# Kernel tuning notes

Measured on AMD Instinct MI355X. Metric: run time of the kernel, lower is better.

Reference implementation:

```python
import jax, jax.numpy as jnp
import numpy as np

OUT_FEATURES = 4096
IN_FEATURES = 4096
GROUP_SIZE = 128
NUM_GROUPS = OUT_FEATURES // GROUP_SIZE  # groups along output-channel axis (axis=0)


def _unpack_int8_to_int4(packed, num_elements):
    # Each int8 byte holds two signed int4 values: low nibble first, then high nibble.
    p = packed.astype(jnp.int8)
    low = jnp.right_shift(jnp.left_shift(p, 4), 4)   # sign-extended low nibble, in [-8, 7]
    high = jnp.right_shift(p, 4)                      # arithmetic shift -> sign-extended high nibble
    vals = jnp.stack([low, high], axis=-1).reshape(-1)
    return vals[:num_elements]


def _dequantize_weight(packed_weight, scales, zero_points):
    int4 = _unpack_int8_to_int4(packed_weight, OUT_FEATURES * IN_FEATURES)
    w = int4.astype(jnp.float32).reshape(NUM_GROUPS, GROUP_SIZE, IN_FEATURES)
    # per-group (over output channels): (q - zp) * scale
    w = (w - zero_points[:, None, None]) * scales[:, None, None]
    return w.reshape(OUT_FEATURES, IN_FEATURES)


def setup_inputs() -> dict:
    key = jax.random.key(0)
    k_x, k_w, k_s, k_zp, k_b = jax.random.split(key, 5)
    x = jax.random.normal(k_x, (8192, IN_FEATURES), dtype=jnp.float32)
    # packed int4 weights stored as signed bytes
    packed_weight = jax.random.randint(k_w, (OUT_FEATURES * IN_FEATURES // 2,), 0, 256, dtype=jnp.int32) - 128
    scales = jax.random.uniform(k_s, (NUM_GROUPS,), dtype=jnp.float32) * 0.02 + 0.001
    zero_points = jax.random.normal(k_zp, (NUM_GROUPS,), dtype=jnp.float32) * 0.5
    bias = jax.random.normal(k_b, (OUT_FEATURES,), dtype=jnp.float32)
    return {"x": x, "packed_weight": packed_weight, "scales": scales,
            "zero_points": zero_points, "bias": bias}


def reference(x, packed_weight, scales, zero_points, bias):
    weight = _dequantize_weight(packed_weight, scales, zero_points)  # [out, in]
    return jnp.einsum('bi,oi->bo', x, weight) + bias
```

## Files before the change

### kernel.cpp

```cpp
#include <hip/hip_runtime.h>
#include <cstdint>
#include <cstddef>

#define M_DIM 8192
#define N_DIM 4096
#define K_DIM 4096
#define CHUNK_M 4096

typedef __attribute__((ext_vector_type(8))) short bf16x8;
typedef __attribute__((ext_vector_type(4))) float floatx4;

__device__ __forceinline__ ushort f2bf_rne(float f) {
    union { float f; uint32_t u; } a;
    a.f = f;
    uint32_t u = a.u;
    uint32_t r = (u + 0x7fffu + ((u >> 16) & 1u)) >> 16;
    return (ushort)r;
}

__device__ __forceinline__ uint32_t pk_bf_trunc(float f0, float f1) {
    return __builtin_amdgcn_perm(__float_as_uint(f1), __float_as_uint(f0),
                                 0x07060302u);
}

__global__ void dequant_w_kernel(const int4* __restrict__ pw,
                                 const float* __restrict__ scales,
                                 const float* __restrict__ zps,
                                 uint4* __restrict__ wb, int np4) {
    int p4 = blockIdx.x * blockDim.x + threadIdx.x;
    if (p4 >= np4) return;
    int p = p4 * 4;
    int g = p >> 18;
    float s = scales[g];
    float b = -zps[g] * s;
    int4 v = pw[p4];
    int vv[4] = { v.x, v.y, v.z, v.w };
    ushort o[8];
#pragma unroll
    for (int j = 0; j < 4; ++j) {
        int lo = ((int)((uint32_t)vv[j] << 28)) >> 28;
        int hi = ((int)((uint32_t)vv[j] << 24)) >> 28;
        o[2 * j]     = f2bf_rne(fmaf((float)lo, s, b));
        o[2 * j + 1] = f2bf_rne(fmaf((float)hi, s, b));
    }
    uint4 st;
    st.x = (uint32_t)o[0] | ((uint32_t)o[1] << 16);
    st.y = (uint32_t)o[2] | ((uint32_t)o[3] << 16);
    st.z = (uint32_t)o[4] | ((uint32_t)o[5] << 16);
    st.w = (uint32_t)o[6] | ((uint32_t)o[7] << 16);
    wb[p4] = st;
}

__global__ void convert_x_kernel(const float4* __restrict__ x4,
                                 ushort4* __restrict__ out4, int n4) {
    int i = blockIdx.x * blockDim.x + threadIdx.x;
    if (i >= n4) return;
    float4 v = x4[i];
    ushort4 o;
    o.x = f2bf_rne(v.x);
    o.y = f2bf_rne(v.y);
    o.z = f2bf_rne(v.z);
    o.w = f2bf_rne(v.w);
    out4[i] = o;
}

#define TBM 256
#define TBN 256
#define TBK 32
#define NT  (K_DIM / TBK)
#define A_E 8192
#define SLOT_E 16384

__global__ __launch_bounds__(512, 2)
void gemm_bf16_256(const ushort* __restrict__ A,
                   const ushort* __restrict__ B,
                   const float* __restrict__ bias,
                   float* __restrict__ C) {
    __shared__ ushort lds[4 * SLOT_E];

    const int tid  = threadIdx.x;
    const int lane = tid & 63;
    const int wave = tid >> 6;
    const int wm   = wave >> 2;
    const int wn   = wave & 3;

    const int nwg = gridDim.x;
    const int cpx = nwg >> 3;
    const int bid = blockIdx.x;
    const int swz = (bid & 7) * cpx + (bid >> 3);
    const int bn  = swz & (N_DIM / TBN - 1);
    const int bm  = swz / (N_DIM / TBN);

    const ushort* Ab = A + (size_t)(bm * TBM) * K_DIM;
    const ushort* Bb = B + (size_t)(bn * TBN) * K_DIM;

    const int srow = tid >> 2;
    const int scol = (((tid & 3) ^ ((tid >> 3) & 3)) * 8);
    const ushort* gA0 = Ab + (size_t)srow * K_DIM + scol;
    const ushort* gA1 = gA0 + (size_t)128 * K_DIM;
    const ushort* gB0 = Bb + (size_t)srow * K_DIM + scol;
    const ushort* gB1 = gB0 + (size_t)128 * K_DIM;
    const int wdst = wave * 512;

    const int frow = lane & 15;
    const int fcol = (((lane >> 4) ^ ((frow >> 1) & 3)) * 8);
    const int aoff = (wm * 128 + frow) * TBK + fcol;
    const int boff = A_E + (wn * 64 + frow) * TBK + fcol;

    floatx4 acc[8][4] = {};

#define STAGE_A(tt)                                                           \
    {                                                                          \
        const int k0s = ((tt) & (NT - 1)) * TBK;                               \
        ushort* d = lds + ((tt) & 3) * SLOT_E + wdst;                          \
        __builtin_amdgcn_global_load_lds(                                      \
            (const __attribute__((address_space(1))) void*)(gA0 + k0s),        \
            (__attribute__((address_space(3))) void*)d, 16, 0, 0);             \
        __builtin_amdgcn_global_load_lds(                                      \
            (const __attribute__((address_space(1))) void*)(gA1 + k0s),        \
            (__attribute__((address_space(3))) void*)(d + 4096), 16, 0, 0);    \
    }
#define STAGE_B(tt)                                                           \
    {                                                                          \
        const int k0s = ((tt) & (NT - 1)) * TBK;                               \
        ushort* d = lds + ((tt) & 3) * SLOT_E + A_E + wdst;                    \
        __builtin_amdgcn_global_load_lds(                                      \
            (const __attribute__((address_space(1))) void*)(gB0 + k0s),        \
            (__attribute__((address_space(3))) void*)d, 16, 0, 0);             \
        __builtin_amdgcn_global_load_lds(                                      \
            (const __attribute__((address_space(1))) void*)(gB1 + k0s),        \
            (__attribute__((address_space(3))) void*)(d + 4096), 16, 0, 0);    \
    }

#define BODY(T, afc, bfc, afn, bfn)                                           \
    {                                                                          \
        const ushort* bcur = lds + ((T) & 3) * SLOT_E;                         \
        const ushort* bnxt = lds + (((T) + 1) & 3) * SLOT_E;                   \
        bf16x8 afb[4];                                                         \
                                             \
        _Pragma("unroll")                                                      \
        for (int i = 0; i < 4; ++i)                                            \
            afb[i] = *(const bf16x8*)(bcur + aoff + (4 + i) * 512);            \
        STAGE_A((T) + 3)                                                       \
        __builtin_amdgcn_sched_barrier(0);                                     \
        __builtin_amdgcn_s_setprio(1);                                         \
        _Pragma("unroll")                                                      \
        for (int i = 0; i < 2; ++i)                                            \
            _Pragma("unroll")                                                  \
            for (int j = 0; j < 4; ++j)                                        \
                acc[i][j] = __builtin_amdgcn_mfma_f32_16x16x32_bf16(           \
                    afc[i], bfc[j], acc[i][j], 0, 0, 0);                       \
        __builtin_amdgcn_s_setprio(0);                                         \
        __builtin_amdgcn_sched_barrier(0);                                     \
                                             \
        _Pragma("unroll")                                                      \
        for (int j = 0; j < 4; ++j)                                            \
            bfn[j] = *(const bf16x8*)(bnxt + boff + j * 512);                  \
        STAGE_B((T) + 3)                                                       \
        __builtin_amdgcn_sched_barrier(0);                                     \
        __builtin_amdgcn_s_setprio(1);                                         \
        _Pragma("unroll")                                                      \
        for (int i = 2; i < 4; ++i)                                            \
            _Pragma("unroll")                                                  \
            for (int j = 0; j < 4; ++j)                                        \
                acc[i][j] = __builtin_amdgcn_mfma_f32_16x16x32_bf16(           \
                    afc[i], bfc[j], acc[i][j], 0, 0, 0);                       \
        __builtin_amdgcn_s_setprio(0);                                         \
        __builtin_amdgcn_sched_barrier(0);                                     \
                                                            \
        _Pragma("unroll")                                                      \
        for (int i = 0; i < 4; ++i)                                            \
            afn[i] = *(const bf16x8*)(bnxt + aoff + i * 512);                  \
        __builtin_amdgcn_sched_barrier(0);                                     \
                \
        asm volatile("s_waitcnt lgkmcnt(8)" ::: "memory");                     \
        __builtin_amdgcn_sched_barrier(0);                                     \
        __builtin_amdgcn_s_setprio(1);                                         \
        _Pragma("unroll")                                                      \
        for (int i = 0; i < 2; ++i)                                            \
            _Pragma("unroll")                                                  \
            for (int j = 0; j < 4; ++j)                                        \
                acc[4 + i][j] = __builtin_amdgcn_mfma_f32_16x16x32_bf16(       \
                    afb[i], bfc[j], acc[4 + i][j], 0, 0, 0);                   \
        __builtin_amdgcn_s_setprio(0);                                         \
        __builtin_amdgcn_sched_barrier(0);                                     \
        __builtin_amdgcn_s_setprio(1);                                         \
        _Pragma("unroll")                                                      \
        for (int i = 2; i < 4; ++i)                                            \
            _Pragma("unroll")                                                  \
            for (int j = 0; j < 4; ++j)                                        \
                acc[4 + i][j] = __builtin_amdgcn_mfma_f32_16x16x32_bf16(       \
                    afb[i], bfc[j], acc[4 + i][j], 0, 0, 0);                   \
        __builtin_amdgcn_s_setprio(0);                                         \
        asm volatile("s_waitcnt vmcnt(4)" ::: "memory");                       \
        __builtin_amdgcn_s_barrier();                                          \
        __builtin_amdgcn_sched_barrier(0);                                     \
    }

    STAGE_A(0) STAGE_B(0)
    STAGE_A(1) STAGE_B(1)
    STAGE_A(2) STAGE_B(2)
    asm volatile("s_waitcnt vmcnt(4)" ::: "memory");
    __builtin_amdgcn_s_barrier();
    __builtin_amdgcn_sched_barrier(0);

    bf16x8 af0[4], bf0[4], af1[4], bf1[4];
#pragma unroll
    for (int j = 0; j < 4; ++j)
        bf0[j] = *(const bf16x8*)(lds + boff + j * 512);
#pragma unroll
    for (int i = 0; i < 4; ++i)
        af0[i] = *(const bf16x8*)(lds + aoff + i * 512);

    for (int t = 0; t < NT; t += 2) {
        BODY(t,     af0, bf0, af1, bf1)
        BODY(t + 1, af1, bf1, af0, bf0)
    }
#undef BODY
#undef STAGE_A
#undef STAGE_B

    const int crow0 = bm * TBM + wm * 128;
    const int ccol0 = bn * TBN + wn * 64;
    const int rl = lane >> 4;
    const int cl = lane & 15;
#pragma unroll
    for (int j = 0; j < 4; ++j) {
        const int col = ccol0 + j * 16 + cl;
        const float bv = bias[col];
#pragma unroll
        for (int i = 0; i < 8; ++i) {
            const int row = crow0 + i * 16 + rl * 4;
            float* cp = C + (size_t)row * N_DIM + col;
#pragma unroll
            for (int r = 0; r < 4; ++r)
                cp[(size_t)r * N_DIM] = acc[i][j][r] + bv;
        }
    }
}

#define BM 128
#define BN 128
#define BK 32

__global__ void gemm_fused_kernel(const float* __restrict__ X,
                                  const ushort* __restrict__ B,
                                  const float* __restrict__ bias,
                                  float* __restrict__ C) {
    __shared__ ushort As[BM * BK];
    __shared__ ushort Bs[BN * BK];

    const int tid  = threadIdx.x;
    const int lane = tid & 63;
    const int wave = tid >> 6;
    const int wm   = wave >> 1;
    const int wn   = wave & 1;
    const int bm   = blockIdx.y;
    const int bn   = blockIdx.x;

    const int ar = tid >> 2;
    const int ac = (tid & 3) * 8;
    const float* xp0 = X + (size_t)(bm * BM + ar) * K_DIM + ac;
    const float* xp1 = xp0 + (size_t)64 * K_DIM;
    ushort* as0 = As + ar * BK + ac;
    ushort* as1 = as0 + 64 * BK;

    const int scol = (lane & 3) * 8;
    const ushort* Bb = B + (size_t)(bn * BN) * K_DIM;

    floatx4 acc[4][4] = {};

    for (int k0 = 0; k0 < K_DIM; k0 += BK) {
        float4 a0 = *(const float4*)(xp0 + k0);
        float4 a1 = *(const float4*)(xp0 + k0 + 4);
        float4 b0 = *(const float4*)(xp1 + k0);
        float4 b1 = *(const float4*)(xp1 + k0 + 4);
#pragma unroll
        for (int q = 0; q < 2; ++q) {
            const int chunk = wave * 2 + q;
            const int r = chunk * 16 + (lane >> 2);
            const ushort* gb = Bb + (size_t)r * K_DIM + k0 + scol;
            __builtin_amdgcn_global_load_lds(
                (const __attribute__((address_space(1))) void*)gb,
                (__attribute__((address_space(3))) void*)(Bs + chunk * 512),
                16, 0, 0);
        }
        uint4 w0, w1;
        w0.x = pk_bf_trunc(a0.x, a0.y);
        w0.y = pk_bf_trunc(a0.z, a0.w);
        w0.z = pk_bf_trunc(a1.x, a1.y);
        w0.w = pk_bf_trunc(a1.z, a1.w);
        w1.x = pk_bf_trunc(b0.x, b0.y);
        w1.y = pk_bf_trunc(b0.z, b0.w);
        w1.z = pk_bf_trunc(b1.x, b1.y);
        w1.w = pk_bf_trunc(b1.z, b1.w);
        *(uint4*)as0 = w0;
        *(uint4*)as1 = w1;

        __syncthreads();

        bf16x8 af[4], bfr[4];
        const int frow = lane & 15;
        const int fcol = (lane >> 4) * 8;
#pragma unroll
        for (int i = 0; i < 4; ++i) {
            af[i]  = *(const bf16x8*)(As + (wm * 64 + i * 16 + frow) * BK + fcol);
            bfr[i] = *(const bf16x8*)(Bs + (wn * 64 + i * 16 + frow) * BK + fcol);
        }
#pragma unroll
        for (int i = 0; i < 4; ++i)
#pragma unroll
            for (int j = 0; j < 4; ++j)
                acc[i][j] = __builtin_amdgcn_mfma_f32_16x16x32_bf16(
                    af[i], bfr[j], acc[i][j], 0, 0, 0);
        __syncthreads();
    }

    const int crow0 = bm * BM + wm * 64;
    const int ccol0 = bn * BN + wn * 64;
    const int rl = lane >> 4;
    const int cl = lane & 15;
#pragma unroll
    for (int j = 0; j < 4; ++j) {
        const int col = ccol0 + j * 16 + cl;
        const float bv = bias[col];
#pragma unroll
        for (int i = 0; i < 4; ++i) {
            const int row = crow0 + i * 16 + rl * 4;
            float* cp = C + (size_t)row * N_DIM + col;
#pragma unroll
            for (int r = 0; r < 4; ++r)
                cp[(size_t)r * N_DIM] = acc[i][j][r] + bv;
        }
    }
}

extern "C" void kernel_launch(void* const* d_in, const int* in_sizes, int n_in,
                              void* d_out, int out_size, void* d_ws, size_t ws_size,
                              hipStream_t stream) {
    const float* x      = (const float*)d_in[0];
    const int*   pw     = (const int*)d_in[1];
    const float* scales = (const float*)d_in[2];
    const float* zps    = (const float*)d_in[3];
    const float* bias   = (const float*)d_in[4];
    float* out = (float*)d_out;

    ushort* wb = (ushort*)d_ws;

    {
        int np4 = (N_DIM * K_DIM / 2) / 4;
        dequant_w_kernel<<<np4 / 256, 256, 0, stream>>>(
            (const int4*)pw, scales, zps, (uint4*)wb, np4);
    }

    const size_t need_full  = ((size_t)N_DIM * K_DIM + (size_t)M_DIM * K_DIM) * 2;
    const size_t need_chunk = ((size_t)N_DIM * K_DIM + (size_t)CHUNK_M * K_DIM) * 2;

    if (ws_size >= need_full) {
        ushort* xb = wb + (size_t)N_DIM * K_DIM;
        int n4 = (M_DIM * K_DIM) / 4;
        convert_x_kernel<<<n4 / 256, 256, 0, stream>>>(
            (const float4*)x, (ushort4*)xb, n4);
        int nblk = (M_DIM / TBM) * (N_DIM / TBN);
        gemm_bf16_256<<<nblk, 512, 0, stream>>>(xb, wb, bias, out);
    } else if (ws_size >= need_chunk) {
        ushort* xb = wb + (size_t)N_DIM * K_DIM;
        for (int c = 0; c < M_DIM / CHUNK_M; ++c) {
            const float* xc = x + (size_t)c * CHUNK_M * K_DIM;
            float* oc = out + (size_t)c * CHUNK_M * N_DIM;
            int n4 = (CHUNK_M * K_DIM) / 4;
            convert_x_kernel<<<n4 / 256, 256, 0, stream>>>(
                (const float4*)xc, (ushort4*)xb, n4);
            int nblk = (CHUNK_M / TBM) * (N_DIM / TBN);
            gemm_bf16_256<<<nblk, 512, 0, stream>>>(xb, wb, bias, oc);
        }
    } else {
        dim3 grid(N_DIM / BN, M_DIM / BM);
        gemm_fused_kernel<<<grid, 256, 0, stream>>>(x, wb, bias, out);
    }
}
```

Before: 464.3 us.

## Restructure bf16 GEMM main loop to TBK=64 double-buffered quadrant schedule

Reworks the 256x256 bf16 GEMM from a 4-slot TBK=32 ring into a 2-buffer TBK=64 scheme. Each K tile is split into four MFMA quadrants (A lo/hi by B lo/hi), and the next tile's global-to-LDS loads are interleaved between them. Wave-to-output mapping changes to split rows and columns into two halves, and the LDS swizzle widens to 8 chunks. The aim is fewer barriers per FLOP and more MFMA work per LDS fetch, at the cost of more barriers inside each tile and a shallower prefetch depth.

```diff
diff --git a/kernel.cpp b/kernel.cpp
--- a/kernel.cpp
+++ b/kernel.cpp
@@ -66,17 +66,16 @@
 
 #define TBM 256
 #define TBN 256
-#define TBK 32
-#define NT  (K_DIM / TBK)
-#define A_E 8192
-#define SLOT_E 16384
+#define TBK 64
+#define NKT (K_DIM / TBK)
+#define BUF_E 32768
 
 __global__ __launch_bounds__(512, 2)
 void gemm_bf16_256(const ushort* __restrict__ A,
                    const ushort* __restrict__ B,
                    const float* __restrict__ bias,
                    float* __restrict__ C) {
-    __shared__ ushort lds[4 * SLOT_E];
+    __shared__ ushort lds[2 * BUF_E];
 
     const int tid  = threadIdx.x;
     const int lane = tid & 63;
@@ -94,143 +93,149 @@
     const ushort* Ab = A + (size_t)(bm * TBM) * K_DIM;
     const ushort* Bb = B + (size_t)(bn * TBN) * K_DIM;
 
-    const int srow = tid >> 2;
-    const int scol = (((tid & 3) ^ ((tid >> 3) & 3)) * 8);
-    const ushort* gA0 = Ab + (size_t)srow * K_DIM + scol;
-    const ushort* gA1 = gA0 + (size_t)128 * K_DIM;
-    const ushort* gB0 = Bb + (size_t)srow * K_DIM + scol;
-    const ushort* gB1 = gB0 + (size_t)128 * K_DIM;
-    const int wdst = wave * 512;
+    const int r0 = tid >> 3;
+    const int kc = ((tid & 7) ^ (r0 & 7)) * 8;
+    const ushort* gA = Ab + (size_t)r0 * K_DIM + kc;
+    const ushort* gB = Bb + (size_t)r0 * K_DIM + kc;
+    const int sdst = tid * 8;
 
     const int frow = lane & 15;
-    const int fcol = (((lane >> 4) ^ ((frow >> 1) & 3)) * 8);
-    const int aoff = (wm * 128 + frow) * TBK + fcol;
-    const int boff = A_E + (wn * 64 + frow) * TBK + fcol;
+    const int col0 = (((lane >> 4) ^ (frow & 7)) * 8);
+    const int lbA = wm * 4096 + frow * 64;
+    const int lbB = 16384 + wn * 2048 + frow * 64;
+    const int colx[2] = { col0, col0 ^ 32 };
 
     floatx4 acc[8][4] = {};
 
-#define STAGE_A(tt)                                                           \
+#define STAGE(SBUF, TS, OFFE, ROWOFF)                                         \
     {                                                                          \
-        const int k0s = ((tt) & (NT - 1)) * TBK;                               \
-        ushort* d = lds + ((tt) & 3) * SLOT_E + wdst;                          \
+        const int k0s = ((TS) & (NKT - 1)) * TBK;                              \
+        ushort* d = (ushort*)lds + (SBUF) * BUF_E + (OFFE) + sdst;             \
+        const ushort* g = ((OFFE) >= 16384 ? gB : gA);                         \
         __builtin_amdgcn_global_load_lds(                                      \
-            (const __attribute__((address_space(1))) void*)(gA0 + k0s),        \
+            (const __attribute__((address_space(1))) void*)                    \
+                (g + (size_t)(ROWOFF) * K_DIM + k0s),                          \
             (__attribute__((address_space(3))) void*)d, 16, 0, 0);             \
         __builtin_amdgcn_global_load_lds(                                      \
-            (const __attribute__((address_space(1))) void*)(gA1 + k0s),        \
+            (const __attribute__((address_space(1))) void*)                    \
+                (g + (size_t)((ROWOFF) + 64) * K_DIM + k0s),                   \
             (__attribute__((address_space(3))) void*)(d + 4096), 16, 0, 0);    \
     }
-#define STAGE_B(tt)                                                           \
+
+#define MFMA_Q(ILO, AFR, JLO, BFR)                                            \
+    _Pragma("unroll")                                                          \
+    for (int i = 0; i < 4; ++i)                                                \
+        _Pragma("unroll")                                                      \
+        for (int j = 0; j < 2; ++j)                                            \
+            _Pragma("unroll")                                                  \
+            for (int ks = 0; ks < 2; ++ks)                                     \
+                acc[(ILO) + i][(JLO) + j] =                                    \
+                    __builtin_amdgcn_mfma_f32_16x16x32_bf16(                   \
+                        AFR[i][ks], BFR[j][ks], acc[(ILO) + i][(JLO) + j],     \
+                        0, 0, 0);
+
+#define TILE(T, CBUF)                                                         \
     {                                                                          \
-        const int k0s = ((tt) & (NT - 1)) * TBK;                               \
-        ushort* d = lds + ((tt) & 3) * SLOT_E + A_E + wdst;                    \
-        __builtin_amdgcn_global_load_lds(                                      \
-            (const __attribute__((address_space(1))) void*)(gB0 + k0s),        \
-            (__attribute__((address_space(3))) void*)d, 16, 0, 0);             \
-        __builtin_amdgcn_global_load_lds(                                      \
-            (const __attribute__((address_space(1))) void*)(gB1 + k0s),        \
-            (__attribute__((address_space(3))) void*)(d + 4096), 16, 0, 0);    \
-    }
-
-#define BODY(T, afc, bfc, afn, bfn)                                           \
-    {                                                                          \
-        const ushort* bcur = lds + ((T) & 3) * SLOT_E;                         \
-        const ushort* bnxt = lds + (((T) + 1) & 3) * SLOT_E;                   \
-        bf16x8 afb[4];                                                         \
-                                             \
+        bf16x8 alo[4][2], ahi[4][2], blo[2][2], bhi[2][2];                     \
+                                                         \
         _Pragma("unroll")                                                      \
         for (int i = 0; i < 4; ++i)                                            \
-            afb[i] = *(const bf16x8*)(bcur + aoff + (4 + i) * 512);            \
-        STAGE_A((T) + 3)                                                       \
+            _Pragma("unroll")                                                  \
+            for (int ks = 0; ks < 2; ++ks)                                     \
+                alo[i][ks] = *(const bf16x8*)(lds + (CBUF) * BUF_E + lbA +     \
+                                              i * 1024 + colx[ks]);            \
+        _Pragma("unroll")                                                      \
+        for (int j = 0; j < 2; ++j)                                            \
+            _Pragma("unroll")                                                  \
+            for (int ks = 0; ks < 2; ++ks)                                     \
+                blo[j][ks] = *(const bf16x8*)(lds + (CBUF) * BUF_E + lbB +     \
+                                              j * 1024 + colx[ks]);            \
+        STAGE((CBUF) ^ 1, (T) + 1, 0, 0)                                       \
+        asm volatile("s_waitcnt lgkmcnt(8)" ::: "memory");                     \
+        __builtin_amdgcn_s_barrier();                                          \
+        asm volatile("s_waitcnt lgkmcnt(0)" ::: "memory");                     \
         __builtin_amdgcn_sched_barrier(0);                                     \
         __builtin_amdgcn_s_setprio(1);                                         \
-        _Pragma("unroll")                                                      \
-        for (int i = 0; i < 2; ++i)                                            \
-            _Pragma("unroll")                                                  \
-            for (int j = 0; j < 4; ++j)                                        \
-                acc[i][j] = __builtin_amdgcn_mfma_f32_16x16x32_bf16(           \
-                    afc[i], bfc[j], acc[i][j], 0, 0, 0);                       \
-        __builtin_amdgcn_s_setprio(0);                                         \
-        __builtin_amdgcn_sched_barrier(0);                                     \
-                                             \
-        _Pragma("unroll")                                                      \
-        for (int j = 0; j < 4; ++j)                                            \
-            bfn[j] = *(const bf16x8*)(bnxt + boff + j * 512);                  \
-        STAGE_B((T) + 3)                                                       \
-        __builtin_amdgcn_sched_barrier(0);                                     \
-        __builtin_amdgcn_s_setprio(1);                                         \
-        _Pragma("unroll")                                                      \
-        for (int i = 2; i < 4; ++i)                                            \
-            _Pragma("unroll")                                                  \
-            for (int j = 0; j < 4; ++j)                                        \
-                acc[i][j] = __builtin_amdgcn_mfma_f32_16x16x32_bf16(           \
-                    afc[i], bfc[j], acc[i][j], 0, 0, 0);                       \
-        __builtin_amdgcn_s_setprio(0);                                         \
-        __builtin_amdgcn_sched_barrier(0);                                     \
-                                                            \
-        _Pragma("unroll")                                                      \
-        for (int i = 0; i < 4; ++i)                                            \
-            afn[i] = *(const bf16x8*)(bnxt + aoff + i * 512);                  \
-        __builtin_amdgcn_sched_barrier(0);                                     \
-                \
-        asm volatile("s_waitcnt lgkmcnt(8)" ::: "memory");                     \
-        __builtin_amdgcn_sched_barrier(0);                                     \
-        __builtin_amdgcn_s_setprio(1);                                         \
-        _Pragma("unroll")                                                      \
-        for (int i = 0; i < 2; ++i)                                            \
-            _Pragma("unroll")                                                  \
-            for (int j = 0; j < 4; ++j)                                        \
-                acc[4 + i][j] = __builtin_amdgcn_mfma_f32_16x16x32_bf16(       \
-                    afb[i], bfc[j], acc[4 + i][j], 0, 0, 0);                   \
-        __builtin_amdgcn_s_setprio(0);                                         \
-        __builtin_amdgcn_sched_barrier(0);                                     \
-        __builtin_amdgcn_s_setprio(1);                                         \
-        _Pragma("unroll")                                                      \
-        for (int i = 2; i < 4; ++i)                                            \
-            _Pragma("unroll")                                                  \
-            for (int j = 0; j < 4; ++j)                                        \
-                acc[4 + i][j] = __builtin_amdgcn_mfma_f32_16x16x32_bf16(       \
-                    afb[i], bfc[j], acc[4 + i][j], 0, 0, 0);                   \
+        MFMA_Q(0, alo, 0, blo)                                                 \
         __builtin_amdgcn_s_setprio(0);                                         \
         asm volatile("s_waitcnt vmcnt(4)" ::: "memory");                       \
         __builtin_amdgcn_s_barrier();                                          \
         __builtin_amdgcn_sched_barrier(0);                                     \
-    }
-
-    STAGE_A(0) STAGE_B(0)
-    STAGE_A(1) STAGE_B(1)
-    STAGE_A(2) STAGE_B(2)
+                                                         \
+        _Pragma("unroll")                                                      \
+        for (int j = 0; j < 2; ++j)                                            \
+            _Pragma("unroll")                                                  \
+            for (int ks = 0; ks < 2; ++ks)                                     \
+                bhi[j][ks] = *(const bf16x8*)(lds + (CBUF) * BUF_E + lbB +     \
+                                              8192 + j * 1024 + colx[ks]);     \
+        STAGE((CBUF) ^ 1, (T) + 1, 16384, 0)                                   \
+        __builtin_amdgcn_s_barrier();                                          \
+        asm volatile("s_waitcnt lgkmcnt(0)" ::: "memory");                     \
+        __builtin_amdgcn_sched_barrier(0);                                     \
+        __builtin_amdgcn_s_setprio(1);                                         \
+        MFMA_Q(0, alo, 2, bhi)                                                 \
+        __builtin_amdgcn_s_setprio(0);                                         \
+        asm volatile("s_waitcnt vmcnt(4)" ::: "memory");                       \
+        __builtin_amdgcn_s_barrier();                                          \
+        __builtin_amdgcn_sched_barrier(0);                                     \
+                                                         \
+        _Pragma("unroll")                                                      \
+        for (int i = 0; i < 4; ++i)                                            \
+            _Pragma("unroll")                                                  \
+            for (int ks = 0; ks < 2; ++ks)                                     \
+                ahi[i][ks] = *(const bf16x8*)(lds + (CBUF) * BUF_E + lbA +     \
+                                              8192 + i * 1024 + colx[ks]);     \
+        STAGE((CBUF) ^ 1, (T) + 1, 24576, 128)                                 \
+        __builtin_amdgcn_s_barrier();                                          \
+        asm volatile("s_waitcnt lgkmcnt(0)" ::: "memory");                     \
+        __builtin_amdgcn_sched_barrier(0);                                     \
+        __builtin_amdgcn_s_setprio(1);                                         \
+        MFMA_Q(4, ahi, 0, blo)                                                 \
+        __builtin_amdgcn_s_setprio(0);                                         \
+        __builtin_amdgcn_s_barrier();                                          \
+        __builtin_amdgcn_sched_barrier(0);                                     \
+                                                         \
+        STAGE((CBUF) ^ 1, (T) + 1, 8192, 128)                                  \
+        __builtin_amdgcn_s_barrier();                                          \
+        __builtin_amdgcn_sched_barrier(0);                                     \
+        __builtin_amdgcn_s_setprio(1);                                         \
+        MFMA_Q(4, ahi, 2, bhi)                                                 \
+        __builtin_amdgcn_s_setprio(0);                                         \
+        asm volatile("s_waitcnt vmcnt(4)" ::: "memory");                       \
+        __builtin_amdgcn_s_barrier();                                          \
+        __builtin_amdgcn_sched_barrier(0);                                     \
+    }
+
+    STAGE(0, 0, 0, 0)
+    STAGE(0, 0, 16384, 0)
+    STAGE(0, 0, 24576, 128)
+    STAGE(0, 0, 8192, 128)
     asm volatile("s_waitcnt vmcnt(4)" ::: "memory");
     __builtin_amdgcn_s_barrier();
     __builtin_amdgcn_sched_barrier(0);
 
-    bf16x8 af0[4], bf0[4], af1[4], bf1[4];
-#pragma unroll
-    for (int j = 0; j < 4; ++j)
-        bf0[j] = *(const bf16x8*)(lds + boff + j * 512);
-#pragma unroll
-    for (int i = 0; i < 4; ++i)
-        af0[i] = *(const bf16x8*)(lds + aoff + i * 512);
-
-    for (int t = 0; t < NT; t += 2) {
-        BODY(t,     af0, bf0, af1, bf1)
-        BODY(t + 1, af1, bf1, af0, bf0)
-    }
-#undef BODY
-#undef STAGE_A
-#undef STAGE_B
-
-    const int crow0 = bm * TBM + wm * 128;
-    const int ccol0 = bn * TBN + wn * 64;
+    for (int t = 0; t < NKT; t += 2) {
+        TILE(t, 0)
+        TILE(t + 1, 1)
+    }
+#undef TILE
+#undef MFMA_Q
+#undef STAGE
+
     const int rl = lane >> 4;
     const int cl = lane & 15;
 #pragma unroll
     for (int j = 0; j < 4; ++j) {
-        const int col = ccol0 + j * 16 + cl;
+        const int col = bn * TBN +
+                        (j < 2 ? wn * 32 + j * 16 : 128 + wn * 32 + (j - 2) * 16) +
+                        cl;
         const float bv = bias[col];
 #pragma unroll
         for (int i = 0; i < 8; ++i) {
-            const int row = crow0 + i * 16 + rl * 4;
+            const int row = bm * TBM +
+                            (i < 4 ? wm * 64 + i * 16
+                                   : 128 + wm * 64 + (i - 4) * 16) +
+                            rl * 4;
             float* cp = C + (size_t)row * N_DIM + col;
 #pragma unroll
             for (int r = 0; r < 4; ++r)
```

After: 459.3 us. Within noise of the previous version (-1.1%).

## Fuse fp32-to-bf16 activation conversion into the 256x256 GEMM pipeline

Applied to the files above, without the earlier changes.

Removes the separate convert_x kernel and the bf16 copy of x. The GEMM now loads fp32 x straight from global memory into registers, converts it with v_cvt_pk_bf16_f32, and writes it into swizzled LDS, interleaved with the asynchronous B tile loads. This drops a full read and write pass over the 128MB activation and a kernel launch. In exchange the GEMM reads twice as many A bytes per tile through registers instead of direct-to-LDS loads, which adds VGPR pressure and vmcnt synchronisation inside the pipelined main loop. The workspace-size fallback paths are also removed.

```diff
diff --git a/kernel.cpp b/kernel.cpp
--- a/kernel.cpp
+++ b/kernel.cpp
@@ -5,7 +5,6 @@
 #define M_DIM 8192
 #define N_DIM 4096
 #define K_DIM 4096
-#define CHUNK_M 4096
 
 typedef __attribute__((ext_vector_type(8))) short bf16x8;
 typedef __attribute__((ext_vector_type(4))) float floatx4;
@@ -18,9 +17,10 @@
     return (ushort)r;
 }
 
-__device__ __forceinline__ uint32_t pk_bf_trunc(float f0, float f1) {
-    return __builtin_amdgcn_perm(__float_as_uint(f1), __float_as_uint(f0),
-                                 0x07060302u);
+__device__ __forceinline__ uint32_t cvtpk_bf16(float lo, float hi) {
+    uint32_t r;
+    asm("v_cvt_pk_bf16_f32 %0, %1, %2" : "=v"(r) : "v"(lo), "v"(hi));
+    return r;
 }
 
 __global__ void dequant_w_kernel(const int4* __restrict__ pw,
@@ -51,19 +51,6 @@
     wb[p4] = st;
 }
 
-__global__ void convert_x_kernel(const float4* __restrict__ x4,
-                                 ushort4* __restrict__ out4, int n4) {
-    int i = blockIdx.x * blockDim.x + threadIdx.x;
-    if (i >= n4) return;
-    float4 v = x4[i];
-    ushort4 o;
-    o.x = f2bf_rne(v.x);
-    o.y = f2bf_rne(v.y);
-    o.z = f2bf_rne(v.z);
-    o.w = f2bf_rne(v.w);
-    out4[i] = o;
-}
-
 #define TBM 256
 #define TBN 256
 #define TBK 32
@@ -72,10 +59,10 @@
 #define SLOT_E 16384
 
 __global__ __launch_bounds__(512, 2)
-void gemm_bf16_256(const ushort* __restrict__ A,
-                   const ushort* __restrict__ B,
-                   const float* __restrict__ bias,
-                   float* __restrict__ C) {
+void gemm_fused_256(const float* __restrict__ X,
+                    const ushort* __restrict__ B,
+                    const float* __restrict__ bias,
+                    float* __restrict__ C) {
     __shared__ ushort lds[4 * SLOT_E];
 
     const int tid  = threadIdx.x;
@@ -91,16 +78,20 @@
     const int bn  = swz & (N_DIM / TBN - 1);
     const int bm  = swz / (N_DIM / TBN);
 
-    const ushort* Ab = A + (size_t)(bm * TBM) * K_DIM;
     const ushort* Bb = B + (size_t)(bn * TBN) * K_DIM;
 
     const int srow = tid >> 2;
-    const int scol = (((tid & 3) ^ ((tid >> 3) & 3)) * 8);
-    const ushort* gA0 = Ab + (size_t)srow * K_DIM + scol;
-    const ushort* gA1 = gA0 + (size_t)128 * K_DIM;
-    const ushort* gB0 = Bb + (size_t)srow * K_DIM + scol;
+    const int scolB = (((tid & 3) ^ ((tid >> 3) & 3)) * 8);
+    const ushort* gB0 = Bb + (size_t)srow * K_DIM + scolB;
     const ushort* gB1 = gB0 + (size_t)128 * K_DIM;
     const int wdst = wave * 512;
+
+    const int wrow = tid >> 1;
+    const int wh   = tid & 1;
+    const int wq   = (wrow >> 1) & 3;
+    const int we1  = wrow * TBK + (((2 * wh) ^ wq) * 8);
+    const int we2  = we1 ^ 8;
+    const float* gX = X + (size_t)(bm * TBM + wrow) * K_DIM + wh * 16;
 
     const int frow = lane & 15;
     const int fcol = (((lane >> 4) ^ ((frow >> 1) & 3)) * 8);
@@ -108,22 +99,31 @@
     const int boff = A_E + (wn * 64 + frow) * TBK + fcol;
 
     floatx4 acc[8][4] = {};
-
-#define STAGE_A(tt)                                                           \
+    float4 rA0, rA1, rA2, rA3;
+
+#define LOAD_A(tt)                                                            \
+    {                                                                          \
+        const int k0n = ((tt) & (NT - 1)) * TBK;                               \
+        rA0 = *(const float4*)(gX + k0n);                                      \
+        rA1 = *(const float4*)(gX + k0n + 4);                                  \
+        rA2 = *(const float4*)(gX + k0n + 8);                                  \
+        rA3 = *(const float4*)(gX + k0n + 12);                                 \
+    }
+#define WRITE_A(tt)                                                           \
+    {                                                                          \
+        ushort* wp = (ushort*)lds + ((tt) & 3) * SLOT_E;                       \
+        uint4 v1, v2;                                                          \
+        v1.x = cvtpk_bf16(rA0.x, rA0.y); v1.y = cvtpk_bf16(rA0.z, rA0.w);      \
+        v1.z = cvtpk_bf16(rA1.x, rA1.y); v1.w = cvtpk_bf16(rA1.z, rA1.w);      \
+        v2.x = cvtpk_bf16(rA2.x, rA2.y); v2.y = cvtpk_bf16(rA2.z, rA2.w);      \
+        v2.z = cvtpk_bf16(rA3.x, rA3.y); v2.w = cvtpk_bf16(rA3.z, rA3.w);      \
+        *(uint4*)(wp + we1) = v1;                                              \
+        *(uint4*)(wp + we2) = v2;                                              \
+    }
+#define STAGE_B(tt)                                                           \
     {                                                                          \
         const int k0s = ((tt) & (NT - 1)) * TBK;                               \
-        ushort* d = lds + ((tt) & 3) * SLOT_E + wdst;                          \
-        __builtin_amdgcn_global_load_lds(                                      \
-            (const __attribute__((address_space(1))) void*)(gA0 + k0s),        \
-            (__attribute__((address_space(3))) void*)d, 16, 0, 0);             \
-        __builtin_amdgcn_global_load_lds(                                      \
-            (const __attribute__((address_space(1))) void*)(gA1 + k0s),        \
-            (__attribute__((address_space(3))) void*)(d + 4096), 16, 0, 0);    \
-    }
-#define STAGE_B(tt)                                                           \
-    {                                                                          \
-        const int k0s = ((tt) & (NT - 1)) * TBK;                               \
-        ushort* d = lds + ((tt) & 3) * SLOT_E + A_E + wdst;                    \
+        ushort* d = (ushort*)lds + ((tt) & 3) * SLOT_E + A_E + wdst;           \
         __builtin_amdgcn_global_load_lds(                                      \
             (const __attribute__((address_space(1))) void*)(gB0 + k0s),        \
             (__attribute__((address_space(3))) void*)d, 16, 0, 0);             \
@@ -134,14 +134,20 @@
 
 #define BODY(T, afc, bfc, afn, bfn)                                           \
     {                                                                          \
+                \
+        asm volatile("s_waitcnt vmcnt(2)" ::: "memory");                       \
+        __builtin_amdgcn_sched_barrier(0);                                     \
+        WRITE_A((T) + 2)                                                       \
+        LOAD_A((T) + 3)                                                        \
+        __builtin_amdgcn_sched_barrier(0);                                     \
         const ushort* bcur = lds + ((T) & 3) * SLOT_E;                         \
         const ushort* bnxt = lds + (((T) + 1) & 3) * SLOT_E;                   \
         bf16x8 afb[4];                                                         \
-                                             \
+                                                  \
         _Pragma("unroll")                                                      \
         for (int i = 0; i < 4; ++i)                                            \
             afb[i] = *(const bf16x8*)(bcur + aoff + (4 + i) * 512);            \
-        STAGE_A((T) + 3)                                                       \
+        STAGE_B((T) + 3)                                                       \
         __builtin_amdgcn_sched_barrier(0);                                     \
         __builtin_amdgcn_s_setprio(1);                                         \
         _Pragma("unroll")                                                      \
@@ -152,11 +158,10 @@
                     afc[i], bfc[j], acc[i][j], 0, 0, 0);                       \
         __builtin_amdgcn_s_setprio(0);                                         \
         __builtin_amdgcn_sched_barrier(0);                                     \
-                                             \
+                                                            \
         _Pragma("unroll")                                                      \
         for (int j = 0; j < 4; ++j)                                            \
             bfn[j] = *(const bf16x8*)(bnxt + boff + j * 512);                  \
-        STAGE_B((T) + 3)                                                       \
         __builtin_amdgcn_sched_barrier(0);                                     \
         __builtin_amdgcn_s_setprio(1);                                         \
         _Pragma("unroll")                                                      \
@@ -172,7 +177,8 @@
         for (int i = 0; i < 4; ++i)                                            \
             afn[i] = *(const bf16x8*)(bnxt + aoff + i * 512);                  \
         __builtin_amdgcn_sched_barrier(0);                                     \
-                \
+        \
+         \
         asm volatile("s_waitcnt lgkmcnt(8)" ::: "memory");                     \
         __builtin_amdgcn_sched_barrier(0);                                     \
         __builtin_amdgcn_s_setprio(1);                                         \
@@ -192,15 +198,20 @@
                 acc[4 + i][j] = __builtin_amdgcn_mfma_f32_16x16x32_bf16(       \
                     afb[i], bfc[j], acc[4 + i][j], 0, 0, 0);                   \
         __builtin_amdgcn_s_setprio(0);                                         \
-        asm volatile("s_waitcnt vmcnt(4)" ::: "memory");                       \
         __builtin_amdgcn_s_barrier();                                          \
         __builtin_amdgcn_sched_barrier(0);                                     \
     }
 
-    STAGE_A(0) STAGE_B(0)
-    STAGE_A(1) STAGE_B(1)
-    STAGE_A(2) STAGE_B(2)
+    LOAD_A(0)
+    asm volatile("s_waitcnt vmcnt(0)" ::: "memory");
+    WRITE_A(0)
+    LOAD_A(1)
+    asm volatile("s_waitcnt vmcnt(0)" ::: "memory");
+    WRITE_A(1)
+    LOAD_A(2)
+    STAGE_B(0) STAGE_B(1) STAGE_B(2)
     asm volatile("s_waitcnt vmcnt(4)" ::: "memory");
+    asm volatile("s_waitcnt lgkmcnt(0)" ::: "memory");
     __builtin_amdgcn_s_barrier();
     __builtin_amdgcn_sched_barrier(0);
 
@@ -217,8 +228,9 @@
         BODY(t + 1, af1, bf1, af0, bf0)
     }
 #undef BODY
-#undef STAGE_A
 #undef STAGE_B
+#undef WRITE_A
+#undef LOAD_A
 
     const int crow0 = bm * TBM + wm * 128;
     const int ccol0 = bn * TBN + wn * 64;
@@ -230,102 +242,6 @@
         const float bv = bias[col];
 #pragma unroll
         for (int i = 0; i < 8; ++i) {
-            const int row = crow0 + i * 16 + rl * 4;
-            float* cp = C + (size_t)row * N_DIM + col;
-#pragma unroll
-            for (int r = 0; r < 4; ++r)
-                cp[(size_t)r * N_DIM] = acc[i][j][r] + bv;
-        }
-    }
-}
-
-#define BM 128
-#define BN 128
-#define BK 32
-
-__global__ void gemm_fused_kernel(const float* __restrict__ X,
-                                  const ushort* __restrict__ B,
-                                  const float* __restrict__ bias,
-                                  float* __restrict__ C) {
-    __shared__ ushort As[BM * BK];
-    __shared__ ushort Bs[BN * BK];
-
-    const int tid  = threadIdx.x;
-    const int lane = tid & 63;
-    const int wave = tid >> 6;
-    const int wm   = wave >> 1;
-    const int wn   = wave & 1;
-    const int bm   = blockIdx.y;
-    const int bn   = blockIdx.x;
-
-    const int ar = tid >> 2;
-    const int ac = (tid & 3) * 8;
-    const float* xp0 = X + (size_t)(bm * BM + ar) * K_DIM + ac;
-    const float* xp1 = xp0 + (size_t)64 * K_DIM;
-    ushort* as0 = As + ar * BK + ac;
-    ushort* as1 = as0 + 64 * BK;
-
-    const int scol = (lane & 3) * 8;
-    const ushort* Bb = B + (size_t)(bn * BN) * K_DIM;
-
-    floatx4 acc[4][4] = {};
-
-    for (int k0 = 0; k0 < K_DIM; k0 += BK) {
-        float4 a0 = *(const float4*)(xp0 + k0);
-        float4 a1 = *(const float4*)(xp0 + k0 + 4);
-        float4 b0 = *(const float4*)(xp1 + k0);
-        float4 b1 = *(const float4*)(xp1 + k0 + 4);
-#pragma unroll
-        for (int q = 0; q < 2; ++q) {
-            const int chunk = wave * 2 + q;
-            const int r = chunk * 16 + (lane >> 2);
-            const ushort* gb = Bb + (size_t)r * K_DIM + k0 + scol;
-            __builtin_amdgcn_global_load_lds(
-                (const __attribute__((address_space(1))) void*)gb,
-                (__attribute__((address_space(3))) void*)(Bs + chunk * 512),
-                16, 0, 0);
-        }
-        uint4 w0, w1;
-        w0.x = pk_bf_trunc(a0.x, a0.y);
-        w0.y = pk_bf_trunc(a0.z, a0.w);
-        w0.z = pk_bf_trunc(a1.x, a1.y);
-        w0.w = pk_bf_trunc(a1.z, a1.w);
-        w1.x = pk_bf_trunc(b0.x, b0.y);
-        w1.y = pk_bf_trunc(b0.z, b0.w);
-        w1.z = pk_bf_trunc(b1.x, b1.y);
-        w1.w = pk_bf_trunc(b1.z, b1.w);
-        *(uint4*)as0 = w0;
-        *(uint4*)as1 = w1;
-
-        __syncthreads();
-
-        bf16x8 af[4], bfr[4];
-        const int frow = lane & 15;
-        const int fcol = (lane >> 4) * 8;
-#pragma unroll
-        for (int i = 0; i < 4; ++i) {
-            af[i]  = *(const bf16x8*)(As + (wm * 64 + i * 16 + frow) * BK + fcol);
-            bfr[i] = *(const bf16x8*)(Bs + (wn * 64 + i * 16 + frow) * BK + fcol);
-        }
-#pragma unroll
-        for (int i = 0; i < 4; ++i)
-#pragma unroll
-            for (int j = 0; j < 4; ++j)
-                acc[i][j] = __builtin_amdgcn_mfma_f32_16x16x32_bf16(
-                    af[i], bfr[j], acc[i][j], 0, 0, 0);
-        __syncthreads();
-    }
-
-    const int crow0 = bm * BM + wm * 64;
-    const int ccol0 = bn * BN + wn * 64;
-    const int rl = lane >> 4;
-    const int cl = lane & 15;
-#pragma unroll
-    for (int j = 0; j < 4; ++j) {
-        const int col = ccol0 + j * 16 + cl;
-        const float bv = bias[col];
-#pragma unroll
-        for (int i = 0; i < 4; ++i) {
             const int row = crow0 + i * 16 + rl * 4;
             float* cp = C + (size_t)row * N_DIM + col;
 #pragma unroll
@@ -353,29 +269,6 @@
             (const int4*)pw, scales, zps, (uint4*)wb, np4);
     }
 
-    const size_t need_full  = ((size_t)N_DIM * K_DIM + (size_t)M_DIM * K_DIM) * 2;
-    const size_t need_chunk = ((size_t)N_DIM * K_DIM + (size_t)CHUNK_M * K_DIM) * 2;
-
-    if (ws_size >= need_full) {
-        ushort* xb = wb + (size_t)N_DIM * K_DIM;
-        int n4 = (M_DIM * K_DIM) / 4;
-        convert_x_kernel<<<n4 / 256, 256, 0, stream>>>(
-            (const float4*)x, (ushort4*)xb, n4);
-        int nblk = (M_DIM / TBM) * (N_DIM / TBN);
-        gemm_bf16_256<<<nblk, 512, 0, stream>>>(xb, wb, bias, out);
-    } else if (ws_size >= need_chunk) {
-        ushort* xb = wb + (size_t)N_DIM * K_DIM;
-        for (int c = 0; c < M_DIM / CHUNK_M; ++c) {
-            const float* xc = x + (size_t)c * CHUNK_M * K_DIM;
-            float* oc = out + (size_t)c * CHUNK_M * N_DIM;
-            int n4 = (CHUNK_M * K_DIM) / 4;
-            convert_x_kernel<<<n4 / 256, 256, 0, stream>>>(
-                (const float4*)xc, (ushort4*)xb, n4);
-            int nblk = (CHUNK_M / TBM) * (N_DIM / TBN);
-            gemm_bf16_256<<<nblk, 512, 0, stream>>>(xb, wb, bias, oc);
-        }
-    } else {
-        dim3 grid(N_DIM / BN, M_DIM / BM);
-        gemm_fused_kernel<<<grid, 256, 0, stream>>>(x, wb, bias, out);
-    }
-}
+    int nblk = (M_DIM / TBM) * (N_DIM / TBN);
+    gemm_fused_256<<<nblk, 512, 0, stream>>>(x, wb, bias, out);
+}
```

New measurement: 615.9 us. 32.6% more time.
